# Optimization experiments

Hardware: AMD Instinct MI355X
Metric: run time of the kernel (lower is better)

The kernel has to match this reference:

```python
import jax, jax.numpy as jnp
import numpy as np

N, IN_FEAT, OUT_FEAT = 8192, 512, 256
SLOPE = 0.1


def setup_inputs() -> dict:
    key = jax.random.key(0)
    k1, k2, k3, k4, k5 = jax.random.split(key, 5)
    doc = jax.random.normal(k1, (N, IN_FEAT), dtype=jnp.float32)
    W = jax.random.normal(k2, (IN_FEAT, OUT_FEAT), dtype=jnp.float32) * (1.0 / np.sqrt(IN_FEAT))
    W_b = jax.random.normal(k3, (OUT_FEAT,), dtype=jnp.float32) * 0.01
    a = jax.random.normal(k4, (2 * OUT_FEAT,), dtype=jnp.float32) * (1.0 / np.sqrt(2 * OUT_FEAT))
    a_b = jax.random.normal(k5, (1,), dtype=jnp.float32) * 0.01
    return {"doc": doc, "W": W, "W_b": W_b, "a": a, "a_b": a_b}


def reference(doc, W, W_b, a, a_b):
    # h = W(doc): [N, outFeat]
    h = doc @ W + W_b
    d = h.shape[-1]
    # aParams(cat(h_i, h_j)) = a1.h_i + a2.h_j + b  (avoids the O(N^2*2d) concat)
    a1, a2 = a[:d], a[d:]
    score = (h @ a1)[:, None] + (h @ a2)[None, :] + a_b[0]  # [N, N]
    score = jax.nn.leaky_relu(score, SLOPE)
    # adj=None path -> all-ones mask, the where() is a no-op
    att = jax.nn.softmax(score, axis=1)  # normalize over neighbors j
    out = jax.nn.leaky_relu(att @ h, SLOPE)  # [N, outFeat]
    return out, att
```

## Files before the change

kernel.cpp:

```cpp
#include <hip/hip_runtime.h>
#include <hip/hip_bf16.h>


typedef __attribute__((ext_vector_type(4))) float f32x4;
typedef __attribute__((ext_vector_type(8))) short short8;
typedef __attribute__((ext_vector_type(4))) unsigned short ushort4v;

#define SLOPE 0.1f
#define NROW 8192
#define DDIM 256

__device__ __forceinline__ float lrelu(float x){ return fmaxf(x, SLOPE * x); }

__device__ __forceinline__ unsigned short f2bf(float f){
  union { float f; unsigned u; } v; v.f = f;
  unsigned r = (v.u + 0x7fffu + ((v.u >> 16) & 1u)) >> 16;
  return (unsigned short)r;
}
__device__ __forceinline__ float bf2f(unsigned short u){
  union { unsigned u; float f; } v; v.u = (unsigned)u << 16; return v.f;
}
__device__ __forceinline__ unsigned cvt_pk_bf16(float lo, float hi){
  unsigned r;
  asm("v_cvt_pk_bf16_f32 %0, %1, %2" : "=v"(r) : "v"(lo), "v"(hi));
  return r;
}

__global__ __launch_bounds__(256) void k_prep(
    const float* __restrict__ W,
    unsigned short* __restrict__ Wt_hi, unsigned short* __restrict__ Wt_lo)
{
  const int tid = blockIdx.x * 256 + threadIdx.x;
  const int c = tid >> 7, kq = tid & 127;
  ushort4v hi, lo;
#pragma unroll
  for (int j = 0; j < 4; ++j) {
    const float v = W[(size_t)(kq * 4 + j) * 256 + c];
    hi[j] = f2bf(v);
    lo[j] = f2bf(v - bf2f(hi[j]));
  }
  *reinterpret_cast<ushort4v*>(Wt_hi + (size_t)c * 512 + kq * 4) = hi;
  *reinterpret_cast<ushort4v*>(Wt_lo + (size_t)c * 512 + kq * 4) = lo;
}

__global__ __launch_bounds__(512, 2) void k_h(
    const float* __restrict__ doc, const unsigned short* __restrict__ Wt_hi,
    const unsigned short* __restrict__ Wt_lo, const float* __restrict__ Wb,
    const float* __restrict__ a,
    unsigned short* __restrict__ ht, float* __restrict__ s1,
    float* __restrict__ e2, float* __restrict__ e02)
{
  __shared__ __align__(16) short8 aH[2][2][64];
  __shared__ __align__(16) short8 aL[2][2][64];
  __shared__ float sred[8][2][32];

  const int t = threadIdx.x, w = t >> 6, l = t & 63;
  const int lr = l & 15, lg = l >> 4;
  const int rb = blockIdx.x * 32;
  const int cb = w * 32;

  f32x4 acc[2][2];
#pragma unroll
  for (int rt = 0; rt < 2; ++rt)
#pragma unroll
    for (int ct = 0; ct < 2; ++ct) acc[rt][ct] = (f32x4){0.f, 0.f, 0.f, 0.f};

  const float* docp = doc + (size_t)(rb + w * 16 + lr) * 512 + lg * 8;

  f32x4 v0, v1;
  auto loadDoc = [&](int k0) { if (w < 2) {
      v0 = *reinterpret_cast<const f32x4*>(docp + k0);
      v1 = *reinterpret_cast<const f32x4*>(docp + k0 + 4);
  }};
  auto writeStage = [&](int pb) { if (w < 2) {
      union { short8 v; unsigned short u[8]; } hi, lo;
#pragma unroll
      for (int q = 0; q < 4; ++q) {
        hi.u[q] = f2bf(v0[q]);     lo.u[q] = f2bf(v0[q] - bf2f(hi.u[q]));
        hi.u[4+q] = f2bf(v1[q]);   lo.u[4+q] = f2bf(v1[q] - bf2f(hi.u[4+q]));
      }
      aH[pb][w][l] = hi.v;
      aL[pb][w][l] = lo.v;
  }};

  loadDoc(0); writeStage(0); loadDoc(32);

  for (int n = 0; n < 16; ++n) {
    const int kk = n * 32;
    const int par = n & 1;

    asm volatile("s_waitcnt lgkmcnt(0)\n\ts_barrier" ::: "memory");

    const short8 ah0 = aH[par][0][l];
    const short8 ah1 = aH[par][1][l];
    const short8 al0 = aL[par][0][l];
    const short8 al1 = aL[par][1][l];

    short8 bh[2], bl[2];
#pragma unroll
    for (int ct = 0; ct < 2; ++ct) {
      const size_t off = (size_t)(cb + ct * 16 + lr) * 512 + kk + lg * 8;
      bh[ct] = *reinterpret_cast<const short8*>(Wt_hi + off);
      bl[ct] = *reinterpret_cast<const short8*>(Wt_lo + off);
    }

    if (n + 1 < 16) writeStage(par ^ 1);
    if (n + 2 < 16) loadDoc((n + 2) * 32);

#pragma unroll
    for (int ct = 0; ct < 2; ++ct) {
      acc[0][ct] = __builtin_amdgcn_mfma_f32_16x16x32_bf16(ah0, bh[ct], acc[0][ct], 0, 0, 0);
      acc[1][ct] = __builtin_amdgcn_mfma_f32_16x16x32_bf16(ah1, bh[ct], acc[1][ct], 0, 0, 0);
      acc[0][ct] = __builtin_amdgcn_mfma_f32_16x16x32_bf16(ah0, bl[ct], acc[0][ct], 0, 0, 0);
      acc[1][ct] = __builtin_amdgcn_mfma_f32_16x16x32_bf16(ah1, bl[ct], acc[1][ct], 0, 0, 0);
      acc[0][ct] = __builtin_amdgcn_mfma_f32_16x16x32_bf16(al0, bh[ct], acc[0][ct], 0, 0, 0);
      acc[1][ct] = __builtin_amdgcn_mfma_f32_16x16x32_bf16(al1, bh[ct], acc[1][ct], 0, 0, 0);
    }
  }

  float bias[2];
#pragma unroll
  for (int ct = 0; ct < 2; ++ct) bias[ct] = Wb[cb + ct * 16 + lr];
#pragma unroll
  for (int rt = 0; rt < 2; ++rt)
#pragma unroll
    for (int ct = 0; ct < 2; ++ct) {
#pragma unroll
      for (int q = 0; q < 4; ++q) acc[rt][ct][q] += bias[ct];
      ushort4v u;
#pragma unroll
      for (int q = 0; q < 4; ++q) u[q] = f2bf(acc[rt][ct][q]);
      *reinterpret_cast<ushort4v*>(
          ht + (size_t)(cb + ct * 16 + lr) * 8192 + rb + rt * 16 + lg * 4) = u;
    }

  float a1c[2], a2c[2];
#pragma unroll
  for (int ct = 0; ct < 2; ++ct) {
    a1c[ct] = a[cb + ct * 16 + lr];
    a2c[ct] = a[256 + cb + ct * 16 + lr];
  }
  float p1[2][4], p2[2][4];
#pragma unroll
  for (int rt = 0; rt < 2; ++rt)
#pragma unroll
    for (int q = 0; q < 4; ++q) {
      float x1 = 0.f, x2 = 0.f;
#pragma unroll
      for (int ct = 0; ct < 2; ++ct) {
        x1 = fmaf(acc[rt][ct][q], a1c[ct], x1);
        x2 = fmaf(acc[rt][ct][q], a2c[ct], x2);
      }
#pragma unroll
      for (int off = 1; off < 16; off <<= 1) {
        x1 += __shfl_xor(x1, off);
        x2 += __shfl_xor(x2, off);
      }
      p1[rt][q] = x1; p2[rt][q] = x2;
    }
  __syncthreads();
  if (lr == 0) {
#pragma unroll
    for (int rt = 0; rt < 2; ++rt)
#pragma unroll
      for (int q = 0; q < 4; ++q) {
        sred[w][0][rt * 16 + lg * 4 + q] = p1[rt][q];
        sred[w][1][rt * 16 + lg * 4 + q] = p2[rt][q];
      }
  }
  __syncthreads();
  if (t < 32) {
    float v1s = 0.f, v2s = 0.f;
#pragma unroll
    for (int ww = 0; ww < 8; ++ww) { v1s += sred[ww][0][t]; v2s += sred[ww][1][t]; }
    const int r = rb + t;
    s1[r] = v1s;
    e2[r] = __expf(v2s);
    e02[r] = __expf(SLOPE * v2s);
  }
}

__global__ __launch_bounds__(256) void k_z(
    const float* __restrict__ s1, const float* __restrict__ e2g,
    const float* __restrict__ e02g, const float* __restrict__ abp,
    float* __restrict__ rowinfo)
{
  __shared__ __align__(16) float es[8192];
  __shared__ __align__(16) float fs[8192];
  const int t = threadIdx.x;
  for (int i = t * 4; i < 8192; i += 1024) {
    *reinterpret_cast<f32x4*>(&es[i]) = *reinterpret_cast<const f32x4*>(e2g + i);
    *reinterpret_cast<f32x4*>(&fs[i]) = *reinterpret_cast<const f32x4*>(e02g + i);
  }
  __syncthreads();
  const int w = t >> 6, l = t & 63;
  const float ab = abp[0];
  const int rb = blockIdx.x * 16 + w * 4;
  float T[4], E1[4], E01[4];
#pragma unroll
  for (int rr = 0; rr < 4; ++rr) {
    const float s1a = s1[rb + rr] + ab;
    E1[rr] = __expf(s1a); E01[rr] = __expf(SLOPE * s1a); T[rr] = __expf(-s1a);
  }
  float zA[4] = {0.f,0.f,0.f,0.f}, zB[4] = {0.f,0.f,0.f,0.f};
  for (int i = l * 4; i < 8192; i += 256) {
    const f32x4 e = *reinterpret_cast<const f32x4*>(&es[i]);
    const f32x4 f = *reinterpret_cast<const f32x4*>(&fs[i]);
#pragma unroll
    for (int rr = 0; rr < 4; ++rr)
#pragma unroll
      for (int q = 0; q < 4; ++q) {
        const bool c = (e[q] >= T[rr]);
        zA[rr] += c ? e[q] : 0.f;
        zB[rr] += c ? 0.f : f[q];
      }
  }
#pragma unroll
  for (int rr = 0; rr < 4; ++rr) {
    float z = E1[rr] * zA[rr] + E01[rr] * zB[rr];
#pragma unroll
    for (int off = 32; off > 0; off >>= 1) z += __shfl_down(z, off);
    if (l == 0) {
      const float iz = 1.0f / z;
      f32x4 ri = (f32x4){E1[rr] * iz, E01[rr] * iz, T[rr], iz};
      *reinterpret_cast<f32x4*>(rowinfo + (size_t)(rb + rr) * 4) = ri;
    }
  }
}

__global__ __launch_bounds__(512, 4) void k_att(
    const float* __restrict__ rowinfo, const float* __restrict__ e2g,
    const float* __restrict__ e02g, const unsigned short* __restrict__ ht,
    float* __restrict__ att, float* __restrict__ part, int CHUNK)
{
  extern __shared__ __align__(16) char smem[];
  char* plsb  = smem;
  float* e2s  = reinterpret_cast<float*>(smem + 8192);
  float* e02s = e2s + CHUNK;

  const int t = threadIdx.x, w = t >> 6, l = t & 63;
  const int lr = l & 15, lg = l >> 4;
  const int kbase = blockIdx.x * CHUNK;
  const int rb = blockIdx.y * 64;

  for (int i = t * 4; i < CHUNK; i += 2048) {
    *reinterpret_cast<f32x4*>(e2s + i)  = *reinterpret_cast<const f32x4*>(e2g + kbase + i);
    *reinterpret_cast<f32x4*>(e02s + i) = *reinterpret_cast<const f32x4*>(e02g + kbase + i);
  }

  const int r = l >> 3, jc = l & 7;
  const int rowW = rb + w * 8 + r;
  const f32x4 ri = *reinterpret_cast<const f32x4*>(rowinfo + (size_t)rowW * 4);
  const float E1z = ri[0], E01z = ri[1], T = ri[2];
  float* attW = att + (size_t)rowW * 8192 + kbase + jc * 4;
  const int fragoff = (w >> 1) * 1024 + ((jc >> 1) * 16 + (w & 1) * 8 + r) * 16 + (jc & 1) * 8;

  __syncthreads();

  auto gen = [&](int kw, int pb) {
    const f32x4 eA = *reinterpret_cast<const f32x4*>(e2s + kw + jc * 4);
    const f32x4 fA = *reinterpret_cast<const f32x4*>(e02s + kw + jc * 4);
    f32x4 pA;
#pragma unroll
    for (int q = 0; q < 4; ++q) {
      const bool cA = (eA[q] >= T);
      pA[q] = (cA ? E1z : E01z) * (cA ? eA[q] : fA[q]);
    }
    *reinterpret_cast<f32x4*>(attW + kw) = pA;
    uint2 u;
    u.x = cvt_pk_bf16(pA[0], pA[1]); u.y = cvt_pk_bf16(pA[2], pA[3]);
    *reinterpret_cast<uint2*>(plsb + pb * 4096 + fragoff) = u;
  };

  const unsigned short* hbase = ht + (size_t)(w * 32 + lr) * 8192 + kbase + lg * 8;
  auto loadB = [&](short8* b, int n) {
    const int kk = n * 32;
    b[0] = *reinterpret_cast<const short8*>(hbase + kk);
    b[1] = *reinterpret_cast<const short8*>(hbase + kk + (size_t)16 * 8192);
  };

  f32x4 acc[4][2];
#pragma unroll
  for (int rt = 0; rt < 4; ++rt)
#pragma unroll
    for (int ct = 0; ct < 2; ++ct) acc[rt][ct] = (f32x4){0.f, 0.f, 0.f, 0.f};

  auto mma = [&](const short8* b, const short8& af0, const short8& af1,
                 const short8& af2, const short8& af3) {
    __builtin_amdgcn_s_setprio(1);
    acc[0][0] = __builtin_amdgcn_mfma_f32_16x16x32_bf16(af0, b[0], acc[0][0], 0, 0, 0);
    acc[1][0] = __builtin_amdgcn_mfma_f32_16x16x32_bf16(af1, b[0], acc[1][0], 0, 0, 0);
    acc[2][0] = __builtin_amdgcn_mfma_f32_16x16x32_bf16(af2, b[0], acc[2][0], 0, 0, 0);
    acc[3][0] = __builtin_amdgcn_mfma_f32_16x16x32_bf16(af3, b[0], acc[3][0], 0, 0, 0);
    acc[0][1] = __builtin_amdgcn_mfma_f32_16x16x32_bf16(af0, b[1], acc[0][1], 0, 0, 0);
    acc[1][1] = __builtin_amdgcn_mfma_f32_16x16x32_bf16(af1, b[1], acc[1][1], 0, 0, 0);
    acc[2][1] = __builtin_amdgcn_mfma_f32_16x16x32_bf16(af2, b[1], acc[2][1], 0, 0, 0);
    acc[3][1] = __builtin_amdgcn_mfma_f32_16x16x32_bf16(af3, b[1], acc[3][1], 0, 0, 0);
    __builtin_amdgcn_s_setprio(0);
  };

  short8 bAr[2], bBr[2];
  loadB(bAr, 0);
  gen(0, 0);

  const int NIT = CHUNK / 32;
  const short8* buf0 = reinterpret_cast<const short8*>(plsb);
  const short8* buf1 = reinterpret_cast<const short8*>(plsb + 4096);

  for (int n = 0; n < NIT; n += 2) {
    if (n + 1 < NIT) loadB(bBr, n + 1);
    asm volatile("s_waitcnt lgkmcnt(0)\n\ts_barrier" ::: "memory");
    {
      const short8 af0 = buf0[0 * 64 + l];
      const short8 af1 = buf0[1 * 64 + l];
      const short8 af2 = buf0[2 * 64 + l];
      const short8 af3 = buf0[3 * 64 + l];
      if (n + 1 < NIT) gen((n + 1) * 32, 1);
      mma(bAr, af0, af1, af2, af3);
    }
    if (n + 1 >= NIT) break;
    if (n + 2 < NIT) loadB(bAr, n + 2);
    asm volatile("s_waitcnt lgkmcnt(0)\n\ts_barrier" ::: "memory");
    {
      const short8 af0 = buf1[0 * 64 + l];
      const short8 af1 = buf1[1 * 64 + l];
      const short8 af2 = buf1[2 * 64 + l];
      const short8 af3 = buf1[3 * 64 + l];
      if (n + 2 < NIT) gen((n + 2) * 32, 0);
      mma(bBr, af0, af1, af2, af3);
    }
  }

  float* pb = part + (size_t)blockIdx.x * ((size_t)NROW * DDIM);
#pragma unroll
  for (int rt = 0; rt < 4; ++rt)
#pragma unroll
    for (int ct = 0; ct < 2; ++ct)
#pragma unroll
      for (int q = 0; q < 4; ++q)
        __builtin_nontemporal_store(acc[rt][ct][q],
            pb + (size_t)(rb + rt * 16 + lg * 4 + q) * 256 + w * 32 + ct * 16 + lr);
}

__global__ __launch_bounds__(256) void k_reduce(
    const float* __restrict__ part, float* __restrict__ out, int KS)
{
  const size_t idx = ((size_t)blockIdx.x * 256 + threadIdx.x) * 4;
  f32x4 s = __builtin_nontemporal_load(reinterpret_cast<const f32x4*>(part + idx));
  for (int k = 1; k < KS; ++k) {
    const f32x4 v = __builtin_nontemporal_load(
        reinterpret_cast<const f32x4*>(part + (size_t)k * NROW * DDIM + idx));
#pragma unroll
    for (int q = 0; q < 4; ++q) s[q] += v[q];
  }
#pragma unroll
  for (int q = 0; q < 4; ++q) s[q] = lrelu(s[q]);
  __builtin_nontemporal_store(s, reinterpret_cast<f32x4*>(out + idx));
}

extern "C" void kernel_launch(void* const* d_in, const int* in_sizes, int n_in,
                              void* d_out, int out_size, void* d_ws, size_t ws_size,
                              hipStream_t stream)
{
  const float* doc = (const float*)d_in[0];
  const float* W   = (const float*)d_in[1];
  const float* Wb  = (const float*)d_in[2];
  const float* a   = (const float*)d_in[3];
  const float* ab  = (const float*)d_in[4];

  float* out = (float*)d_out;
  float* att = out + (size_t)8192 * 256;

  char* ws = (char*)d_ws;
  unsigned short* ht    = (unsigned short*)ws;
  unsigned short* Wt_hi = (unsigned short*)(ws + (size_t)4 * 1024 * 1024);
  unsigned short* Wt_lo = Wt_hi + (size_t)256 * 512;
  float* s1      = (float*)(ws + (size_t)4 * 1024 * 1024 + 512 * 1024);
  float* e2      = s1 + 8192;
  float* e02     = e2 + 8192;
  float* rowinfo = e02 + 8192;
  const size_t base = (size_t)5 * 1024 * 1024;
  const size_t partBytes = (size_t)NROW * DDIM * sizeof(float);

  int KS = 1;
  for (int c = 2; c >= 1; c >>= 1)
    if (base + (size_t)c * partBytes <= ws_size) { KS = c; break; }
  float* part = (float*)(ws + base);
  const int CHUNK = NROW / KS;
  const size_t smem = 8192 + (size_t)2 * CHUNK * sizeof(float);

  hipLaunchKernelGGL(k_prep,   dim3(128),     dim3(256), 0,    stream, W, Wt_hi, Wt_lo);
  hipLaunchKernelGGL(k_h,      dim3(256),     dim3(512), 0,    stream, doc, Wt_hi, Wt_lo, Wb, a, ht, s1, e2, e02);
  hipLaunchKernelGGL(k_z,      dim3(512),     dim3(256), 0,    stream, s1, e2, e02, ab, rowinfo);
  hipLaunchKernelGGL(k_att,    dim3(KS, 128), dim3(512), smem, stream, rowinfo, e2, e02, ht, att, part, CHUNK);
  hipLaunchKernelGGL(k_reduce, dim3(2048),    dim3(256), 0,    stream, part, out, KS);
}
```

Baseline: 145.8 us.

## Replace dense att@h matmul with sorted prefix sums over exponential weights

Uses the rank-1 score structure: each attention row is piecewise E1*e2[j] or E01*e02[j] split by a threshold on e2[j]. The columns are sorted by e2 with a counting rank sort, and prefix sums of e2, e02 and of e2*h and e02*h are built in sorted order. Each row's normaliser and output then come from a binary search plus prefix lookups, removing the O(N^2 d) MFMA matmul and the split-K reduction. In exchange it adds several small, mostly serial kernels (a single-block scan, 64-block prefix passes with double accumulation), writes two 8 MB prefix arrays, and a simpler att write kernel.

Measured after the change: 181.1 us. 24.3% more time.

```diff
diff --git a/kernel.cpp b/kernel.cpp
--- a/kernel.cpp
+++ b/kernel.cpp
@@ -4,7 +4,6 @@
 
 typedef __attribute__((ext_vector_type(4))) float f32x4;
 typedef __attribute__((ext_vector_type(8))) short short8;
-typedef __attribute__((ext_vector_type(4))) unsigned short ushort4v;
 
 #define SLOPE 0.1f
 #define NROW 8192
@@ -20,16 +19,12 @@
 __device__ __forceinline__ float bf2f(unsigned short u){
   union { unsigned u; float f; } v; v.u = (unsigned)u << 16; return v.f;
 }
-__device__ __forceinline__ unsigned cvt_pk_bf16(float lo, float hi){
-  unsigned r;
-  asm("v_cvt_pk_bf16_f32 %0, %1, %2" : "=v"(r) : "v"(lo), "v"(hi));
-  return r;
-}
 
 __global__ __launch_bounds__(256) void k_prep(
     const float* __restrict__ W,
     unsigned short* __restrict__ Wt_hi, unsigned short* __restrict__ Wt_lo)
 {
+  typedef __attribute__((ext_vector_type(4))) unsigned short ushort4v;
   const int tid = blockIdx.x * 256 + threadIdx.x;
   const int c = tid >> 7, kq = tid & 127;
   ushort4v hi, lo;
@@ -47,7 +42,7 @@
     const float* __restrict__ doc, const unsigned short* __restrict__ Wt_hi,
     const unsigned short* __restrict__ Wt_lo, const float* __restrict__ Wb,
     const float* __restrict__ a,
-    unsigned short* __restrict__ ht, float* __restrict__ s1,
+    float* __restrict__ h, float* __restrict__ s1,
     float* __restrict__ e2, float* __restrict__ e02)
 {
   __shared__ __align__(16) short8 aH[2][2][64];
@@ -124,15 +119,12 @@
 #pragma unroll
   for (int rt = 0; rt < 2; ++rt)
 #pragma unroll
-    for (int ct = 0; ct < 2; ++ct) {
-#pragma unroll
-      for (int q = 0; q < 4; ++q) acc[rt][ct][q] += bias[ct];
-      ushort4v u;
-#pragma unroll
-      for (int q = 0; q < 4; ++q) u[q] = f2bf(acc[rt][ct][q]);
-      *reinterpret_cast<ushort4v*>(
-          ht + (size_t)(cb + ct * 16 + lr) * 8192 + rb + rt * 16 + lg * 4) = u;
-    }
+    for (int ct = 0; ct < 2; ++ct)
+#pragma unroll
+      for (int q = 0; q < 4; ++q) {
+        acc[rt][ct][q] += bias[ct];
+        h[(size_t)(rb + rt * 16 + lg * 4 + q) * 256 + cb + ct * 16 + lr] = acc[rt][ct][q];
+      }
 
   float a1c[2], a2c[2];
 #pragma unroll
@@ -180,182 +172,187 @@
   }
 }
 
-__global__ __launch_bounds__(256) void k_z(
-    const float* __restrict__ s1, const float* __restrict__ e2g,
-    const float* __restrict__ e02g, const float* __restrict__ abp,
-    float* __restrict__ rowinfo)
-{
-  __shared__ __align__(16) float es[8192];
-  __shared__ __align__(16) float fs[8192];
+__global__ __launch_bounds__(256) void k_sort(
+    const float* __restrict__ e2, const float* __restrict__ e02,
+    int* __restrict__ sortIdx, float* __restrict__ e2srt, float* __restrict__ e02srt)
+{
+  __shared__ __align__(16) float e2L[8192];
   const int t = threadIdx.x;
-  for (int i = t * 4; i < 8192; i += 1024) {
-    *reinterpret_cast<f32x4*>(&es[i]) = *reinterpret_cast<const f32x4*>(e2g + i);
-    *reinterpret_cast<f32x4*>(&fs[i]) = *reinterpret_cast<const f32x4*>(e02g + i);
-  }
+  for (int i = t * 4; i < 8192; i += 1024)
+    *reinterpret_cast<f32x4*>(&e2L[i]) = *reinterpret_cast<const f32x4*>(e2 + i);
   __syncthreads();
-  const int w = t >> 6, l = t & 63;
-  const float ab = abp[0];
-  const int rb = blockIdx.x * 16 + w * 4;
-  float T[4], E1[4], E01[4];
+  const int j = blockIdx.x * 32 + (t >> 3);
+  const int sub = t & 7;
+  const float v = e2L[j];
+  const int k0 = sub * 1024;
+  int cnt = 0;
+  for (int ii = 0; ii < 1024; ii += 4) {
+    const int i = (ii + sub * 132) & 1023;
+    const f32x4 x = *reinterpret_cast<const f32x4*>(&e2L[k0 + i]);
+#pragma unroll
+    for (int q = 0; q < 4; ++q) {
+      const int k = k0 + i + q;
+      cnt += (x[q] > v || (x[q] == v && k < j)) ? 1 : 0;
+    }
+  }
+  cnt += __shfl_down(cnt, 4);
+  cnt += __shfl_down(cnt, 2);
+  cnt += __shfl_down(cnt, 1);
+  if (sub == 0) {
+    sortIdx[cnt] = j;
+    e2srt[cnt] = v;
+    e02srt[cnt] = e02[j];
+  }
+}
+
+__global__ __launch_bounds__(256) void k_scan(
+    const float* __restrict__ e2srt, const float* __restrict__ e02srt,
+    float* __restrict__ pe2, float* __restrict__ pe02)
+{
+  __shared__ double psum[256];
+  const int t = threadIdx.x;
+  for (int pass = 0; pass < 2; ++pass) {
+    const float* src = pass ? e02srt : e2srt;
+    float* dst = pass ? pe02 : pe2;
+    double s = 0;
+    for (int r = t * 32; r < t * 32 + 32; ++r) s += (double)src[r];
+    psum[t] = s;
+    __syncthreads();
+    if (t == 0) {
+      double acc = 0;
+      for (int i = 0; i < 256; ++i) { double tmp = psum[i]; psum[i] = acc; acc += tmp; }
+    }
+    __syncthreads();
+    double acc = psum[t];
+    for (int r = t * 32; r < t * 32 + 32; ++r) { acc += (double)src[r]; dst[r] = (float)acc; }
+    __syncthreads();
+  }
+}
+
+__global__ __launch_bounds__(256) void k_rowinfo(
+    const float* __restrict__ s1, const float* __restrict__ abp,
+    const float* __restrict__ e2srt, const float* __restrict__ pe2,
+    const float* __restrict__ pe02,
+    float* __restrict__ rowinfo, int* __restrict__ cArr)
+{
+  const int i = blockIdx.x * 256 + threadIdx.x;
+  const float s1a = s1[i] + abp[0];
+  const float E1 = __expf(s1a), E01 = __expf(SLOPE * s1a), T = __expf(-s1a);
+  int lo = 0, hi = 8192;
+  while (lo < hi) {
+    const int m = (lo + hi) >> 1;
+    if (e2srt[m] >= T) lo = m + 1; else hi = m;
+  }
+  const int c = lo;
+  const float pe02tot = pe02[8191];
+  const float sum1 = (c > 0) ? pe2[c - 1] : 0.f;
+  const float sum2 = pe02tot - ((c > 0) ? pe02[c - 1] : 0.f);
+  const float Z = E1 * sum1 + E01 * sum2;
+  const float iz = 1.0f / Z;
+  f32x4 ri = (f32x4){E1 * iz, E01 * iz, T, iz};
+  *reinterpret_cast<f32x4*>(rowinfo + (size_t)i * 4) = ri;
+  cArr[i] = c;
+}
+
+__global__ __launch_bounds__(256) void k_segsum(
+    const int* __restrict__ sortIdx, const float* __restrict__ e2srt,
+    const float* __restrict__ e02srt, const float* __restrict__ h,
+    float* __restrict__ seg1, float* __restrict__ seg2)
+{
+  const int s = blockIdx.x, d = threadIdx.x;
+  double a1 = 0, a2 = 0;
+  for (int r = s * 128; r < s * 128 + 128; ++r) {
+    const int j = sortIdx[r];
+    const float hv = h[(size_t)j * 256 + d];
+    a1 += (double)e2srt[r] * hv;
+    a2 += (double)e02srt[r] * hv;
+  }
+  seg1[(size_t)s * 256 + d] = (float)a1;
+  seg2[(size_t)s * 256 + d] = (float)a2;
+}
+
+__global__ __launch_bounds__(256) void k_prefix(
+    const int* __restrict__ sortIdx, const float* __restrict__ e2srt,
+    const float* __restrict__ e02srt, const float* __restrict__ h,
+    const float* __restrict__ seg1, const float* __restrict__ seg2,
+    float* __restrict__ P1, float* __restrict__ P2)
+{
+  const int s = blockIdx.x, d = threadIdx.x;
+  double a1 = 0, a2 = 0;
+  for (int s2 = 0; s2 < s; ++s2) {
+    a1 += (double)seg1[(size_t)s2 * 256 + d];
+    a2 += (double)seg2[(size_t)s2 * 256 + d];
+  }
+  for (int r = s * 128; r < s * 128 + 128; ++r) {
+    const int j = sortIdx[r];
+    const float hv = h[(size_t)j * 256 + d];
+    a1 += (double)e2srt[r] * hv;
+    a2 += (double)e02srt[r] * hv;
+    P1[(size_t)r * 256 + d] = (float)a1;
+    P2[(size_t)r * 256 + d] = (float)a2;
+  }
+}
+
+__global__ __launch_bounds__(256) void k_att(
+    const float* __restrict__ rowinfo, const float* __restrict__ e2g,
+    const float* __restrict__ e02g, float* __restrict__ att)
+{
+  __shared__ __align__(16) float e2s[2048];
+  __shared__ __align__(16) float f2s[2048];
+  __shared__ __align__(16) f32x4 rin[16];
+  const int t = threadIdx.x, w = t >> 6, l = t & 63;
+  const int kbase = blockIdx.x * 2048;
+  const int rb = blockIdx.y * 16;
+  for (int i = t * 4; i < 2048; i += 1024) {
+    *reinterpret_cast<f32x4*>(&e2s[i]) = *reinterpret_cast<const f32x4*>(e2g + kbase + i);
+    *reinterpret_cast<f32x4*>(&f2s[i]) = *reinterpret_cast<const f32x4*>(e02g + kbase + i);
+  }
+  if (t < 16) rin[t] = *reinterpret_cast<const f32x4*>(rowinfo + (size_t)(rb + t) * 4);
+  __syncthreads();
 #pragma unroll
   for (int rr = 0; rr < 4; ++rr) {
-    const float s1a = s1[rb + rr] + ab;
-    E1[rr] = __expf(s1a); E01[rr] = __expf(SLOPE * s1a); T[rr] = __expf(-s1a);
-  }
-  float zA[4] = {0.f,0.f,0.f,0.f}, zB[4] = {0.f,0.f,0.f,0.f};
-  for (int i = l * 4; i < 8192; i += 256) {
-    const f32x4 e = *reinterpret_cast<const f32x4*>(&es[i]);
-    const f32x4 f = *reinterpret_cast<const f32x4*>(&fs[i]);
-#pragma unroll
-    for (int rr = 0; rr < 4; ++rr)
+    const int row = rb + w * 4 + rr;
+    const f32x4 ri = rin[w * 4 + rr];
+    const float E1z = ri[0], E01z = ri[1], T = ri[2];
+    float* ap = att + (size_t)row * 8192 + kbase + l * 4;
+#pragma unroll
+    for (int c = 0; c < 8; ++c) {
+      const int jo = c * 256 + l * 4;
+      const f32x4 e = *reinterpret_cast<const f32x4*>(&e2s[jo]);
+      const f32x4 f = *reinterpret_cast<const f32x4*>(&f2s[jo]);
+      f32x4 p;
 #pragma unroll
       for (int q = 0; q < 4; ++q) {
-        const bool c = (e[q] >= T[rr]);
-        zA[rr] += c ? e[q] : 0.f;
-        zB[rr] += c ? 0.f : f[q];
-      }
-  }
-#pragma unroll
-  for (int rr = 0; rr < 4; ++rr) {
-    float z = E1[rr] * zA[rr] + E01[rr] * zB[rr];
-#pragma unroll
-    for (int off = 32; off > 0; off >>= 1) z += __shfl_down(z, off);
-    if (l == 0) {
-      const float iz = 1.0f / z;
-      f32x4 ri = (f32x4){E1[rr] * iz, E01[rr] * iz, T[rr], iz};
-      *reinterpret_cast<f32x4*>(rowinfo + (size_t)(rb + rr) * 4) = ri;
-    }
-  }
-}
-
-__global__ __launch_bounds__(512, 4) void k_att(
-    const float* __restrict__ rowinfo, const float* __restrict__ e2g,
-    const float* __restrict__ e02g, const unsigned short* __restrict__ ht,
-    float* __restrict__ att, float* __restrict__ part, int CHUNK)
-{
-  extern __shared__ __align__(16) char smem[];
-  char* plsb  = smem;
-  float* e2s  = reinterpret_cast<float*>(smem + 8192);
-  float* e02s = e2s + CHUNK;
-
-  const int t = threadIdx.x, w = t >> 6, l = t & 63;
-  const int lr = l & 15, lg = l >> 4;
-  const int kbase = blockIdx.x * CHUNK;
-  const int rb = blockIdx.y * 64;
-
-  for (int i = t * 4; i < CHUNK; i += 2048) {
-    *reinterpret_cast<f32x4*>(e2s + i)  = *reinterpret_cast<const f32x4*>(e2g + kbase + i);
-    *reinterpret_cast<f32x4*>(e02s + i) = *reinterpret_cast<const f32x4*>(e02g + kbase + i);
-  }
-
-  const int r = l >> 3, jc = l & 7;
-  const int rowW = rb + w * 8 + r;
-  const f32x4 ri = *reinterpret_cast<const f32x4*>(rowinfo + (size_t)rowW * 4);
-  const float E1z = ri[0], E01z = ri[1], T = ri[2];
-  float* attW = att + (size_t)rowW * 8192 + kbase + jc * 4;
-  const int fragoff = (w >> 1) * 1024 + ((jc >> 1) * 16 + (w & 1) * 8 + r) * 16 + (jc & 1) * 8;
-
+        const bool cc = (e[q] >= T);
+        p[q] = (cc ? E1z : E01z) * (cc ? e[q] : f[q]);
+      }
+      *reinterpret_cast<f32x4*>(ap + c * 256) = p;
+    }
+  }
+}
+
+__global__ __launch_bounds__(256) void k_out(
+    const float* __restrict__ rowinfo, const int* __restrict__ cArr,
+    const float* __restrict__ P1, const float* __restrict__ P2,
+    float* __restrict__ out)
+{
+  __shared__ float eL[16], fL[16];
+  __shared__ int cL[16];
+  const int t = threadIdx.x;
+  const int rb = blockIdx.x * 16;
+  if (t < 16) {
+    const f32x4 ri = *reinterpret_cast<const f32x4*>(rowinfo + (size_t)(rb + t) * 4);
+    eL[t] = ri[0]; fL[t] = ri[1]; cL[t] = cArr[rb + t];
+  }
   __syncthreads();
-
-  auto gen = [&](int kw, int pb) {
-    const f32x4 eA = *reinterpret_cast<const f32x4*>(e2s + kw + jc * 4);
-    const f32x4 fA = *reinterpret_cast<const f32x4*>(e02s + kw + jc * 4);
-    f32x4 pA;
-#pragma unroll
-    for (int q = 0; q < 4; ++q) {
-      const bool cA = (eA[q] >= T);
-      pA[q] = (cA ? E1z : E01z) * (cA ? eA[q] : fA[q]);
-    }
-    *reinterpret_cast<f32x4*>(attW + kw) = pA;
-    uint2 u;
-    u.x = cvt_pk_bf16(pA[0], pA[1]); u.y = cvt_pk_bf16(pA[2], pA[3]);
-    *reinterpret_cast<uint2*>(plsb + pb * 4096 + fragoff) = u;
-  };
-
-  const unsigned short* hbase = ht + (size_t)(w * 32 + lr) * 8192 + kbase + lg * 8;
-  auto loadB = [&](short8* b, int n) {
-    const int kk = n * 32;
-    b[0] = *reinterpret_cast<const short8*>(hbase + kk);
-    b[1] = *reinterpret_cast<const short8*>(hbase + kk + (size_t)16 * 8192);
-  };
-
-  f32x4 acc[4][2];
-#pragma unroll
-  for (int rt = 0; rt < 4; ++rt)
-#pragma unroll
-    for (int ct = 0; ct < 2; ++ct) acc[rt][ct] = (f32x4){0.f, 0.f, 0.f, 0.f};
-
-  auto mma = [&](const short8* b, const short8& af0, const short8& af1,
-                 const short8& af2, const short8& af3) {
-    __builtin_amdgcn_s_setprio(1);
-    acc[0][0] = __builtin_amdgcn_mfma_f32_16x16x32_bf16(af0, b[0], acc[0][0], 0, 0, 0);
-    acc[1][0] = __builtin_amdgcn_mfma_f32_16x16x32_bf16(af1, b[0], acc[1][0], 0, 0, 0);
-    acc[2][0] = __builtin_amdgcn_mfma_f32_16x16x32_bf16(af2, b[0], acc[2][0], 0, 0, 0);
-    acc[3][0] = __builtin_amdgcn_mfma_f32_16x16x32_bf16(af3, b[0], acc[3][0], 0, 0, 0);
-    acc[0][1] = __builtin_amdgcn_mfma_f32_16x16x32_bf16(af0, b[1], acc[0][1], 0, 0, 0);
-    acc[1][1] = __builtin_amdgcn_mfma_f32_16x16x32_bf16(af1, b[1], acc[1][1], 0, 0, 0);
-    acc[2][1] = __builtin_amdgcn_mfma_f32_16x16x32_bf16(af2, b[1], acc[2][1], 0, 0, 0);
-    acc[3][1] = __builtin_amdgcn_mfma_f32_16x16x32_bf16(af3, b[1], acc[3][1], 0, 0, 0);
-    __builtin_amdgcn_s_setprio(0);
-  };
-
-  short8 bAr[2], bBr[2];
-  loadB(bAr, 0);
-  gen(0, 0);
-
-  const int NIT = CHUNK / 32;
-  const short8* buf0 = reinterpret_cast<const short8*>(plsb);
-  const short8* buf1 = reinterpret_cast<const short8*>(plsb + 4096);
-
-  for (int n = 0; n < NIT; n += 2) {
-    if (n + 1 < NIT) loadB(bBr, n + 1);
-    asm volatile("s_waitcnt lgkmcnt(0)\n\ts_barrier" ::: "memory");
-    {
-      const short8 af0 = buf0[0 * 64 + l];
-      const short8 af1 = buf0[1 * 64 + l];
-      const short8 af2 = buf0[2 * 64 + l];
-      const short8 af3 = buf0[3 * 64 + l];
-      if (n + 1 < NIT) gen((n + 1) * 32, 1);
-      mma(bAr, af0, af1, af2, af3);
-    }
-    if (n + 1 >= NIT) break;
-    if (n + 2 < NIT) loadB(bAr, n + 2);
-    asm volatile("s_waitcnt lgkmcnt(0)\n\ts_barrier" ::: "memory");
-    {
-      const short8 af0 = buf1[0 * 64 + l];
-      const short8 af1 = buf1[1 * 64 + l];
-      const short8 af2 = buf1[2 * 64 + l];
-      const short8 af3 = buf1[3 * 64 + l];
-      if (n + 2 < NIT) gen((n + 2) * 32, 0);
-      mma(bBr, af0, af1, af2, af3);
-    }
-  }
-
-  float* pb = part + (size_t)blockIdx.x * ((size_t)NROW * DDIM);
-#pragma unroll
-  for (int rt = 0; rt < 4; ++rt)
-#pragma unroll
-    for (int ct = 0; ct < 2; ++ct)
-#pragma unroll
-      for (int q = 0; q < 4; ++q)
-        __builtin_nontemporal_store(acc[rt][ct][q],
-            pb + (size_t)(rb + rt * 16 + lg * 4 + q) * 256 + w * 32 + ct * 16 + lr);
-}
-
-__global__ __launch_bounds__(256) void k_reduce(
-    const float* __restrict__ part, float* __restrict__ out, int KS)
-{
-  const size_t idx = ((size_t)blockIdx.x * 256 + threadIdx.x) * 4;
-  f32x4 s = __builtin_nontemporal_load(reinterpret_cast<const f32x4*>(part + idx));
-  for (int k = 1; k < KS; ++k) {
-    const f32x4 v = __builtin_nontemporal_load(
-        reinterpret_cast<const f32x4*>(part + (size_t)k * NROW * DDIM + idx));
-#pragma unroll
-    for (int q = 0; q < 4; ++q) s[q] += v[q];
-  }
-#pragma unroll
-  for (int q = 0; q < 4; ++q) s[q] = lrelu(s[q]);
-  __builtin_nontemporal_store(s, reinterpret_cast<f32x4*>(out + idx));
+  const float tot2 = P2[(size_t)8191 * 256 + t];
+#pragma unroll 4
+  for (int rr = 0; rr < 16; ++rr) {
+    const int c = cL[rr];
+    const float p1 = (c > 0) ? P1[(size_t)(c - 1) * 256 + t] : 0.f;
+    const float p2 = tot2 - ((c > 0) ? P2[(size_t)(c - 1) * 256 + t] : 0.f);
+    out[(size_t)(rb + rr) * 256 + t] = lrelu(eL[rr] * p1 + fL[rr] * p2);
+  }
 }
 
 extern "C" void kernel_launch(void* const* d_in, const int* in_sizes, int n_in,
@@ -372,26 +369,32 @@
   float* att = out + (size_t)8192 * 256;
 
   char* ws = (char*)d_ws;
-  unsigned short* ht    = (unsigned short*)ws;
-  unsigned short* Wt_hi = (unsigned short*)(ws + (size_t)4 * 1024 * 1024);
-  unsigned short* Wt_lo = Wt_hi + (size_t)256 * 512;
-  float* s1      = (float*)(ws + (size_t)4 * 1024 * 1024 + 512 * 1024);
+  float* h              = (float*)ws;
+  unsigned short* Wt_hi = (unsigned short*)(ws + (size_t)8  * 1024 * 1024);
+  unsigned short* Wt_lo = (unsigned short*)(ws + (size_t)8  * 1024 * 1024 + 262144);
+  char* tb = ws + (size_t)8 * 1024 * 1024 + 524288;
+  float* s1      = (float*)(tb);
   float* e2      = s1 + 8192;
   float* e02     = e2 + 8192;
-  float* rowinfo = e02 + 8192;
-  const size_t base = (size_t)5 * 1024 * 1024;
-  const size_t partBytes = (size_t)NROW * DDIM * sizeof(float);
-
-  int KS = 1;
-  for (int c = 2; c >= 1; c >>= 1)
-    if (base + (size_t)c * partBytes <= ws_size) { KS = c; break; }
-  float* part = (float*)(ws + base);
-  const int CHUNK = NROW / KS;
-  const size_t smem = 8192 + (size_t)2 * CHUNK * sizeof(float);
-
-  hipLaunchKernelGGL(k_prep,   dim3(128),     dim3(256), 0,    stream, W, Wt_hi, Wt_lo);
-  hipLaunchKernelGGL(k_h,      dim3(256),     dim3(512), 0,    stream, doc, Wt_hi, Wt_lo, Wb, a, ht, s1, e2, e02);
-  hipLaunchKernelGGL(k_z,      dim3(512),     dim3(256), 0,    stream, s1, e2, e02, ab, rowinfo);
-  hipLaunchKernelGGL(k_att,    dim3(KS, 128), dim3(512), smem, stream, rowinfo, e2, e02, ht, att, part, CHUNK);
-  hipLaunchKernelGGL(k_reduce, dim3(2048),    dim3(256), 0,    stream, part, out, KS);
-}
+  float* e2srt   = e02 + 8192;
+  float* e02srt  = e2srt + 8192;
+  float* pe2     = e02srt + 8192;
+  float* pe02    = pe2 + 8192;
+  int*   sortIdx = (int*)(pe02 + 8192);
+  int*   cArr    = sortIdx + 8192;
+  float* rowinfo = (float*)(cArr + 8192);
+  float* seg1    = rowinfo + 8192 * 4;
+  float* seg2    = seg1 + 64 * 256;
+  float* P1      = (float*)(ws + (size_t)16 * 1024 * 1024);
+  float* P2      = (float*)(ws + (size_t)24 * 1024 * 1024);
+
+  hipLaunchKernelGGL(k_prep,    dim3(128),      dim3(256), 0, stream, W, Wt_hi, Wt_lo);
+  hipLaunchKernelGGL(k_h,       dim3(256),      dim3(512), 0, stream, doc, Wt_hi, Wt_lo, Wb, a, h, s1, e2, e02);
+  hipLaunchKernelGGL(k_sort,    dim3(256),      dim3(256), 0, stream, e2, e02, sortIdx, e2srt, e02srt);
+  hipLaunchKernelGGL(k_scan,    dim3(1),        dim3(256), 0, stream, e2srt, e02srt, pe2, pe02);
+  hipLaunchKernelGGL(k_rowinfo, dim3(32),       dim3(256), 0, stream, s1, ab, e2srt, pe2, pe02, rowinfo, cArr);
+  hipLaunchKernelGGL(k_segsum,  dim3(64),       dim3(256), 0, stream, sortIdx, e2srt, e02srt, h, seg1, seg2);
+  hipLaunchKernelGGL(k_prefix,  dim3(64),       dim3(256), 0, stream, sortIdx, e2srt, e02srt, h, seg1, seg2, P1, P2);
+  hipLaunchKernelGGL(k_att,     dim3(4, 512),   dim3(256), 0, stream, rowinfo, e2, e02, att);
+  hipLaunchKernelGGL(k_out,     dim3(512),      dim3(256), 0, stream, rowinfo, cArr, P1, P2, out);
+}
```
